# Optimization experiments

Measured on AMD Instinct MI355X. Metric: run time of the kernel, lower is better.

## Reference

```python
import jax, jax.numpy as jnp
import numpy as np

B, T, D, H = 2, 2048, 1024, 16

def setup_inputs() -> dict:
    key = jax.random.key(0)
    k0, k1, k2, k3 = jax.random.split(key, 4)
    s = 0.02
    return {
        "x": jax.random.normal(k0, (B, T, D), dtype=jnp.float32),
        "Wqkv": jax.random.normal(k1, (3 * D, D), dtype=jnp.float32) * s,
        "Wout": jax.random.normal(k2, (D, D), dtype=jnp.float32) * s,
        "bout": jax.random.normal(k3, (D,), dtype=jnp.float32) * s,
    }

def reference(x, Wqkv, Wout, bout):
    b, t, d = x.shape
    h = H
    dh = d // h
    qkv = x @ Wqkv.T  # [b,t,3d]
    q, k, v = jnp.split(qkv, 3, axis=-1)
    def merge_heads(z):
        return z.reshape(b, t, h, dh).transpose(0, 2, 1, 3)  # [b,h,t,dh]
    q, k, v = map(merge_heads, (q, k, v))
    scale = dh ** -0.5
    dots = jnp.einsum('bhid,bhjd->bhij', q, k) * scale  # [b,h,t,t]
    causal_mask = jnp.triu(jnp.ones((t, t), dtype=bool), 1)
    dots = jnp.where(causal_mask, -jnp.inf, dots)
    attn = jax.nn.softmax(dots, axis=-1)
    out = jnp.einsum('bhij,bhjd->bhid', attn, v)  # [b,h,t,dh]
    out = out.transpose(0, 2, 1, 3).reshape(b, t, d)
    return out @ Wout.T + bout
```

## Files before the change

kernel.cpp:

```cpp
#include <hip/hip_runtime.h>
#include <hip/hip_bf16.h>
#include <math.h>

typedef __bf16 bf16x8 __attribute__((ext_vector_type(8)));
typedef float f32x4 __attribute__((ext_vector_type(4)));
typedef unsigned short u16;
typedef unsigned int u32;

#define EXP2F(x) __builtin_amdgcn_exp2f(x)

constexpr int Bz = 2, T = 2048, D = 1024, H = 16;
constexpr int M = Bz * T;
constexpr int NQKV = 3 * D;
constexpr float SCALE2 = 0.125f * 1.44269504089f;

#define GLD_LDS16(g, l) __builtin_amdgcn_global_load_lds( \
    (__attribute__((address_space(1))) void*)(g),          \
    (__attribute__((address_space(3))) void*)(l), 16, 0, 0)

__global__ void f32_to_bf16_kernel(const float* __restrict__ in,
                                   u16* __restrict__ out, int n4) {
  int i = blockIdx.x * blockDim.x + threadIdx.x;
  int stride = gridDim.x * blockDim.x;
  for (; i < n4; i += stride) {
    float4 f = ((const float4*)in)[i];
    ushort4 u;
    u.x = __builtin_bit_cast(u16, (__bf16)f.x);
    u.y = __builtin_bit_cast(u16, (__bf16)f.y);
    u.z = __builtin_bit_cast(u16, (__bf16)f.z);
    u.w = __builtin_bit_cast(u16, (__bf16)f.w);
    ((ushort4*)out)[i] = u;
  }
}

template <bool FP32OUT, bool QSCALE>
__global__ __launch_bounds__(256, 2)
void gemm_bt(const u16* __restrict__ A, const u16* __restrict__ Bm,
             u16* __restrict__ outb, float* __restrict__ outf,
             const float* __restrict__ bias, int K, int ldc) {
  __shared__ __align__(16) u16 sA[128 * 64];
  __shared__ __align__(16) u16 sB[128 * 64];
  const int tid = threadIdx.x;
  const int lane = tid & 63;
  const int wid = tid >> 6;
  const int wr = wid >> 1, wc = wid & 1;

  const int nwg = gridDim.x * gridDim.y;
  const int flat = blockIdx.y * gridDim.x + blockIdx.x;
  const int cpx = nwg >> 3;
  const int swz = (flat & 7) * cpx + (flat >> 3);
  const int bx = swz % gridDim.x;
  const int by = swz / gridDim.x;

  const int row0 = by * 128;
  const int col0 = bx * 128;

  f32x4 acc[4][4];
#pragma unroll
  for (int m = 0; m < 4; ++m)
#pragma unroll
    for (int n = 0; n < 4; ++n) acc[m][n] = (f32x4){0.f, 0.f, 0.f, 0.f};

  const int nk = K >> 6;
  for (int kt = 0; kt < nk; ++kt) {
    const int k0 = kt << 6;
#pragma unroll
    for (int i = 0; i < 4; ++i) {
      int off = i * 4096 + tid * 16;
      int r = off >> 7;
      int cs = (off >> 4) & 7;
      int c = cs ^ (r & 7);
      const u16* ga = A + (size_t)(row0 + r) * K + k0 + c * 8;
      const u16* gb = Bm + (size_t)(col0 + r) * K + k0 + c * 8;
      u16* la = sA + (i * 4096 + (tid & ~63) * 16) / 2;
      u16* lb = sB + (i * 4096 + (tid & ~63) * 16) / 2;
      GLD_LDS16(ga, la);
      GLD_LDS16(gb, lb);
    }
    __syncthreads();
#pragma unroll
    for (int kk = 0; kk < 2; ++kk) {
      bf16x8 af[4], bfv[4];
#pragma unroll
      for (int m = 0; m < 4; ++m) {
        int r = wr * 64 + m * 16 + (lane & 15);
        int cs = (kk * 4 + (lane >> 4)) ^ (r & 7);
        af[m] = *(const bf16x8*)(sA + r * 64 + cs * 8);
      }
#pragma unroll
      for (int n = 0; n < 4; ++n) {
        int r = wc * 64 + n * 16 + (lane & 15);
        int cs = (kk * 4 + (lane >> 4)) ^ (r & 7);
        bfv[n] = *(const bf16x8*)(sB + r * 64 + cs * 8);
      }
#pragma unroll
      for (int m = 0; m < 4; ++m)
#pragma unroll
        for (int n = 0; n < 4; ++n)
          acc[m][n] = __builtin_amdgcn_mfma_f32_16x16x32_bf16(
              af[m], bfv[n], acc[m][n], 0, 0, 0);
    }
    __syncthreads();
  }

  const int orow0 = row0 + wr * 64;
  const int ocol0 = col0 + wc * 64;
#pragma unroll
  for (int m = 0; m < 4; ++m)
#pragma unroll
    for (int n = 0; n < 4; ++n)
#pragma unroll
      for (int j = 0; j < 4; ++j) {
        int rr = orow0 + m * 16 + (lane >> 4) * 4 + j;
        int cc = ocol0 + n * 16 + (lane & 15);
        if (FP32OUT) {
          outf[(size_t)rr * ldc + cc] = acc[m][n][j] + bias[cc];
        } else {
          float v = acc[m][n][j];
          if (QSCALE && cc < D) v *= SCALE2;
          outb[(size_t)rr * ldc + cc] = __builtin_bit_cast(u16, (__bf16)v);
        }
      }
}

__global__ __launch_bounds__(256, 3)
void flash_kernel(const u16* __restrict__ qkv, u16* __restrict__ attn_out) {
  __shared__ __align__(16) u16 sK[2][64 * 64];
  __shared__ __align__(16) u16 sVt[2][64 * 72];
  __shared__ __align__(16) u16 sP[4][16][72];

  const int tid = threadIdx.x;
  const int lane = tid & 63;
  const int l15 = lane & 15;
  const int hi = lane >> 4;
  const int w = tid >> 6;
  const int bh = blockIdx.x;
  const int b = bh >> 4, h = bh & 15;
  const int qt = (gridDim.y - 1) - blockIdx.y;
  const int q0 = qt * 64;
  const int nv = qt + 1;

  const size_t base = (size_t)b * T * 3072;
  const u16* qp = qkv + base + 0 * 1024 + h * 64;
  const u16* kp = qkv + base + 1 * 1024 + h * 64;
  const u16* vp = qkv + base + 2 * 1024 + h * 64;

  ushort4 vr[2][2];
  auto stageK = [&](u16* dst, int kt) {
#pragma unroll
    for (int i = 0; i < 2; ++i) {
      int off = i * 4096 + tid * 16;
      int r = off >> 7;
      int cs = (off >> 4) & 7;
      int c = cs ^ (r & 7);
      GLD_LDS16(kp + (size_t)(kt * 64 + r) * 3072 + c * 8,
                dst + (i * 4096 + (tid & ~63) * 16) / 2);
    }
  };
  auto loadV = [&](int kt) {
#pragma unroll
    for (int i = 0; i < 2; ++i) {
      const u16* gsrc = vp + (size_t)(kt * 64 + lane) * 3072 + (i * 4 + w) * 8;
      vr[i][0] = ((const ushort4*)gsrc)[0];
      vr[i][1] = ((const ushort4*)gsrc)[1];
    }
  };
  auto writeV = [&](u16* dst) {
#pragma unroll
    for (int i = 0; i < 2; ++i) {
      int c = i * 4 + w;
      dst[(c * 8 + 0) * 72 + lane] = vr[i][0].x;
      dst[(c * 8 + 1) * 72 + lane] = vr[i][0].y;
      dst[(c * 8 + 2) * 72 + lane] = vr[i][0].z;
      dst[(c * 8 + 3) * 72 + lane] = vr[i][0].w;
      dst[(c * 8 + 4) * 72 + lane] = vr[i][1].x;
      dst[(c * 8 + 5) * 72 + lane] = vr[i][1].y;
      dst[(c * 8 + 6) * 72 + lane] = vr[i][1].z;
      dst[(c * 8 + 7) * 72 + lane] = vr[i][1].w;
    }
  };

  bf16x8 qf[2];
#pragma unroll
  for (int kk = 0; kk < 2; ++kk)
    qf[kk] = *(const bf16x8*)(qp + (size_t)(q0 + w * 16 + l15) * 3072 +
                              kk * 32 + hi * 8);

  f32x4 o_acc[4];
#pragma unroll
  for (int n = 0; n < 4; ++n) o_acc[n] = (f32x4){0.f, 0.f, 0.f, 0.f};
  float m2 = -INFINITY, l_run = 0.f;

  stageK(sK[0], 0);
  loadV(0);
  writeV(sVt[0]);
  __syncthreads();

  for (int v = 0; v < nv; ++v) {
    const int cur = v & 1;
    const int k0 = v * 64;
    if (v + 1 < nv) {
      stageK(sK[cur ^ 1], v + 1);
      loadV(v + 1);
    }

    bf16x8 kf[2][4];
#pragma unroll
    for (int kk = 0; kk < 2; ++kk)
#pragma unroll
      for (int n = 0; n < 4; ++n) {
        int rk = n * 16 + l15;
        int cs = (kk * 4 + hi) ^ (rk & 7);
        kf[kk][n] = *(const bf16x8*)(&sK[cur][rk * 64 + cs * 8]);
      }

    f32x4 sc[4];
#pragma unroll
    for (int n = 0; n < 4; ++n) sc[n] = (f32x4){0.f, 0.f, 0.f, 0.f};
#pragma unroll
    for (int kk = 0; kk < 2; ++kk)
#pragma unroll
      for (int n = 0; n < 4; ++n)
        sc[n] = __builtin_amdgcn_mfma_f32_16x16x32_bf16(kf[kk][n], qf[kk],
                                                        sc[n], 0, 0, 0);

    const bool diag = (v == nv - 1);
    const int qrow = q0 + w * 16 + l15;
    float mx = -INFINITY;
#pragma unroll
    for (int n = 0; n < 4; ++n)
#pragma unroll
      for (int r = 0; r < 4; ++r) {
        float sv = sc[n][r];
        if (diag) {
          int kpos = k0 + n * 16 + hi * 4 + r;
          if (kpos > qrow) sv = -INFINITY;
        }
        sc[n][r] = sv;
        mx = fmaxf(mx, sv);
      }
    mx = fmaxf(mx, __shfl_xor(mx, 16, 64));
    mx = fmaxf(mx, __shfl_xor(mx, 32, 64));

    const bool skip = __all(mx <= m2);
    float alpha = 1.f;
    if (!skip) {
      float mn = fmaxf(m2, mx);
      alpha = EXP2F(m2 - mn);
      m2 = mn;
    }

    float sum = 0.f;
#pragma unroll
    for (int n = 0; n < 4; ++n) {
      float p0 = EXP2F(sc[n][0] - m2);
      float p1 = EXP2F(sc[n][1] - m2);
      float p2 = EXP2F(sc[n][2] - m2);
      float p3 = EXP2F(sc[n][3] - m2);
      sum += (p0 + p1) + (p2 + p3);
      u32 w01 = ((u32)__builtin_bit_cast(u16, (__bf16)p1) << 16) |
                __builtin_bit_cast(u16, (__bf16)p0);
      u32 w23 = ((u32)__builtin_bit_cast(u16, (__bf16)p3) << 16) |
                __builtin_bit_cast(u16, (__bf16)p2);
      *(u32*)(&sP[w][l15][n * 16 + hi * 4 + 0]) = w01;
      *(u32*)(&sP[w][l15][n * 16 + hi * 4 + 2]) = w23;
    }
    sum += __shfl_xor(sum, 16, 64);
    sum += __shfl_xor(sum, 32, 64);
    l_run = l_run * alpha + sum;

    bf16x8 vf[2][4];
#pragma unroll
    for (int ks = 0; ks < 2; ++ks)
#pragma unroll
      for (int n = 0; n < 4; ++n)
        vf[ks][n] = *(const bf16x8*)(
            &sVt[cur][(n * 16 + l15) * 72 + ks * 32 + hi * 8]);

    if (!skip) {
      float ab[4];
#pragma unroll
      for (int j = 0; j < 4; ++j) ab[j] = __shfl(alpha, hi * 4 + j, 64);
#pragma unroll
      for (int n = 0; n < 4; ++n)
#pragma unroll
        for (int j = 0; j < 4; ++j) o_acc[n][j] *= ab[j];
    }
#pragma unroll
    for (int ks = 0; ks < 2; ++ks) {
      bf16x8 pf = *(const bf16x8*)(&sP[w][l15][ks * 32 + hi * 8]);
#pragma unroll
      for (int n = 0; n < 4; ++n)
        o_acc[n] = __builtin_amdgcn_mfma_f32_16x16x32_bf16(pf, vf[ks][n],
                                                           o_acc[n], 0, 0, 0);
    }

    if (v + 1 < nv) {
      writeV(sVt[cur ^ 1]);
      __syncthreads();
    }
  }

#pragma unroll
  for (int j = 0; j < 4; ++j) {
    float lj = __shfl(l_run, hi * 4 + j, 64);
    float inv = 1.f / lj;
    int row = q0 + w * 16 + hi * 4 + j;
#pragma unroll
    for (int n = 0; n < 4; ++n) {
      int cc = h * 64 + n * 16 + l15;
      attn_out[((size_t)b * T + row) * 1024 + cc] =
          __builtin_bit_cast(u16, (__bf16)(o_acc[n][j] * inv));
    }
  }
}

extern "C" void kernel_launch(void* const* d_in, const int* in_sizes, int n_in,
                              void* d_out, int out_size, void* d_ws,
                              size_t ws_size, hipStream_t stream) {
  (void)in_sizes; (void)n_in; (void)out_size; (void)ws_size;
  const float* x = (const float*)d_in[0];
  const float* Wqkv = (const float*)d_in[1];
  const float* Wout = (const float*)d_in[2];
  const float* bout = (const float*)d_in[3];
  float* out = (float*)d_out;

  char* ws = (char*)d_ws;
  u16* x_bf = (u16*)(ws + 0);
  u16* wqkv_bf = (u16*)(ws + 8388608);
  u16* wout_bf = (u16*)(ws + 14680064);
  u16* qkvb = (u16*)(ws + 16777216);
  u16* aout = (u16*)(ws + 41943040);

  f32_to_bf16_kernel<<<2048, 256, 0, stream>>>(x, x_bf, M * D / 4);
  f32_to_bf16_kernel<<<2048, 256, 0, stream>>>(Wqkv, wqkv_bf, NQKV * D / 4);
  f32_to_bf16_kernel<<<1024, 256, 0, stream>>>(Wout, wout_bf, D * D / 4);

  gemm_bt<false, true><<<dim3(NQKV / 128, M / 128), 256, 0, stream>>>(
      x_bf, wqkv_bf, qkvb, nullptr, nullptr, D, NQKV);

  flash_kernel<<<dim3(Bz * H, T / 64), 256, 0, stream>>>(qkvb, aout);

  gemm_bt<true, false><<<dim3(D / 128, M / 128), 256, 0, stream>>>(
      aout, wout_bf, nullptr, out, bout, D, D);
}
```

Before: 113.4 us.

## Fuse conversion kernels, shuffle P in registers, reorder query tiles, raise occupancy

Merges the three fp32-to-bf16 conversion launches into one kernel. In the flash kernel, the P tile is rearranged into MFMA operand layout with cross-lane shuffles instead of a round trip through LDS, and the sP buffer is removed. Query-tile order is interleaved to balance causal workload, occupancy is raised to 4 blocks per CU, and s_setprio is wrapped around the MFMA sections. The extra shuffles add VALU work and the higher occupancy target may raise register pressure.

```diff
diff --git a/kernel.cpp b/kernel.cpp
--- a/kernel.cpp
+++ b/kernel.cpp
@@ -6,6 +6,7 @@
 typedef float f32x4 __attribute__((ext_vector_type(4)));
 typedef unsigned short u16;
 typedef unsigned int u32;
+typedef u32 u32x4 __attribute__((ext_vector_type(4)));
 
 #define EXP2F(x) __builtin_amdgcn_exp2f(x)
 
@@ -18,18 +19,31 @@
     (__attribute__((address_space(1))) void*)(g),          \
     (__attribute__((address_space(3))) void*)(l), 16, 0, 0)
 
-__global__ void f32_to_bf16_kernel(const float* __restrict__ in,
-                                   u16* __restrict__ out, int n4) {
+__global__ void cvt_all_kernel(const float* __restrict__ x,
+                               const float* __restrict__ wq,
+                               const float* __restrict__ wo,
+                               u16* __restrict__ xb, u16* __restrict__ wqb,
+                               u16* __restrict__ wob) {
+  constexpr int NX = M * D / 4;
+  constexpr int NQ = NQKV * D / 4;
+  constexpr int NW = D * D / 4;
+  constexpr int TOT = NX + NQ + NW;
   int i = blockIdx.x * blockDim.x + threadIdx.x;
   int stride = gridDim.x * blockDim.x;
-  for (; i < n4; i += stride) {
-    float4 f = ((const float4*)in)[i];
+  for (; i < TOT; i += stride) {
+    const float4* src;
+    u16* dst;
+    int j;
+    if (i < NX) { src = (const float4*)x; dst = xb; j = i; }
+    else if (i < NX + NQ) { src = (const float4*)wq; dst = wqb; j = i - NX; }
+    else { src = (const float4*)wo; dst = wob; j = i - NX - NQ; }
+    float4 f = src[j];
     ushort4 u;
     u.x = __builtin_bit_cast(u16, (__bf16)f.x);
     u.y = __builtin_bit_cast(u16, (__bf16)f.y);
     u.z = __builtin_bit_cast(u16, (__bf16)f.z);
     u.w = __builtin_bit_cast(u16, (__bf16)f.w);
-    ((ushort4*)out)[i] = u;
+    ((ushort4*)dst)[j] = u;
   }
 }
 
@@ -123,11 +137,10 @@
       }
 }
 
-__global__ __launch_bounds__(256, 3)
+__global__ __launch_bounds__(256, 4)
 void flash_kernel(const u16* __restrict__ qkv, u16* __restrict__ attn_out) {
   __shared__ __align__(16) u16 sK[2][64 * 64];
   __shared__ __align__(16) u16 sVt[2][64 * 72];
-  __shared__ __align__(16) u16 sP[4][16][72];
 
   const int tid = threadIdx.x;
   const int lane = tid & 63;
@@ -136,7 +149,10 @@
   const int w = tid >> 6;
   const int bh = blockIdx.x;
   const int b = bh >> 4, h = bh & 15;
-  const int qt = (gridDim.y - 1) - blockIdx.y;
+
+  const int yj = blockIdx.y & 7, yg = blockIdx.y >> 3;
+  const int qt = (yg == 0) ? 31 - yj : (yg == 1) ? 16 + yj
+               : (yg == 2) ? 15 - yj : yj;
   const int q0 = qt * 64;
   const int nv = qt + 1;
 
@@ -196,6 +212,10 @@
   writeV(sVt[0]);
   __syncthreads();
 
+  const int idxA = l15 + 32 * (hi & 1);
+  const int idxB = idxA + 16;
+  const bool hiSel = hi >= 2;
+
   for (int v = 0; v < nv; ++v) {
     const int cur = v & 1;
     const int k0 = v * 64;
@@ -217,12 +237,14 @@
     f32x4 sc[4];
 #pragma unroll
     for (int n = 0; n < 4; ++n) sc[n] = (f32x4){0.f, 0.f, 0.f, 0.f};
+    __builtin_amdgcn_s_setprio(1);
 #pragma unroll
     for (int kk = 0; kk < 2; ++kk)
 #pragma unroll
       for (int n = 0; n < 4; ++n)
         sc[n] = __builtin_amdgcn_mfma_f32_16x16x32_bf16(kf[kk][n], qf[kk],
                                                         sc[n], 0, 0, 0);
+    __builtin_amdgcn_s_setprio(0);
 
     const bool diag = (v == nv - 1);
     const int qrow = q0 + w * 16 + l15;
@@ -251,6 +273,7 @@
     }
 
     float sum = 0.f;
+    u32 pp[4][2];
 #pragma unroll
     for (int n = 0; n < 4; ++n) {
       float p0 = EXP2F(sc[n][0] - m2);
@@ -258,17 +281,34 @@
       float p2 = EXP2F(sc[n][2] - m2);
       float p3 = EXP2F(sc[n][3] - m2);
       sum += (p0 + p1) + (p2 + p3);
-      u32 w01 = ((u32)__builtin_bit_cast(u16, (__bf16)p1) << 16) |
-                __builtin_bit_cast(u16, (__bf16)p0);
-      u32 w23 = ((u32)__builtin_bit_cast(u16, (__bf16)p3) << 16) |
-                __builtin_bit_cast(u16, (__bf16)p2);
-      *(u32*)(&sP[w][l15][n * 16 + hi * 4 + 0]) = w01;
-      *(u32*)(&sP[w][l15][n * 16 + hi * 4 + 2]) = w23;
+      pp[n][0] = ((u32)__builtin_bit_cast(u16, (__bf16)p1) << 16) |
+                 __builtin_bit_cast(u16, (__bf16)p0);
+      pp[n][1] = ((u32)__builtin_bit_cast(u16, (__bf16)p3) << 16) |
+                 __builtin_bit_cast(u16, (__bf16)p2);
     }
     sum += __shfl_xor(sum, 16, 64);
     sum += __shfl_xor(sum, 32, 64);
     l_run = l_run * alpha + sum;
 
+    bf16x8 pf[2];
+#pragma unroll
+    for (int ks = 0; ks < 2; ++ks) {
+      u32 a0 = __shfl(pp[2 * ks][0], idxA, 64);
+      u32 b0 = __shfl(pp[2 * ks + 1][0], idxA, 64);
+      u32 a1 = __shfl(pp[2 * ks][1], idxA, 64);
+      u32 b1 = __shfl(pp[2 * ks + 1][1], idxA, 64);
+      u32 a2 = __shfl(pp[2 * ks][0], idxB, 64);
+      u32 b2 = __shfl(pp[2 * ks + 1][0], idxB, 64);
+      u32 a3 = __shfl(pp[2 * ks][1], idxB, 64);
+      u32 b3 = __shfl(pp[2 * ks + 1][1], idxB, 64);
+      u32x4 t;
+      t.x = hiSel ? b0 : a0;
+      t.y = hiSel ? b1 : a1;
+      t.z = hiSel ? b2 : a2;
+      t.w = hiSel ? b3 : a3;
+      pf[ks] = __builtin_bit_cast(bf16x8, t);
+    }
+
     bf16x8 vf[2][4];
 #pragma unroll
     for (int ks = 0; ks < 2; ++ks)
@@ -286,19 +326,17 @@
 #pragma unroll
         for (int j = 0; j < 4; ++j) o_acc[n][j] *= ab[j];
     }
-#pragma unroll
-    for (int ks = 0; ks < 2; ++ks) {
-      bf16x8 pf = *(const bf16x8*)(&sP[w][l15][ks * 32 + hi * 8]);
+    __builtin_amdgcn_s_setprio(1);
+#pragma unroll
+    for (int ks = 0; ks < 2; ++ks)
 #pragma unroll
       for (int n = 0; n < 4; ++n)
-        o_acc[n] = __builtin_amdgcn_mfma_f32_16x16x32_bf16(pf, vf[ks][n],
+        o_acc[n] = __builtin_amdgcn_mfma_f32_16x16x32_bf16(pf[ks], vf[ks][n],
                                                            o_acc[n], 0, 0, 0);
-    }
-
-    if (v + 1 < nv) {
-      writeV(sVt[cur ^ 1]);
-      __syncthreads();
-    }
+    __builtin_amdgcn_s_setprio(0);
+
+    if (v + 1 < nv) writeV(sVt[cur ^ 1]);
+    if (v + 1 < nv) __syncthreads();
   }
 
 #pragma unroll
@@ -332,9 +370,8 @@
   u16* qkvb = (u16*)(ws + 16777216);
   u16* aout = (u16*)(ws + 41943040);
 
-  f32_to_bf16_kernel<<<2048, 256, 0, stream>>>(x, x_bf, M * D / 4);
-  f32_to_bf16_kernel<<<2048, 256, 0, stream>>>(Wqkv, wqkv_bf, NQKV * D / 4);
-  f32_to_bf16_kernel<<<1024, 256, 0, stream>>>(Wout, wout_bf, D * D / 4);
+  cvt_all_kernel<<<2048, 256, 0, stream>>>(x, Wqkv, Wout, x_bf, wqkv_bf,
+                                           wout_bf);
 
   gemm_bt<false, true><<<dim3(NQKV / 128, M / 128), 256, 0, stream>>>(
       x_bf, wqkv_bf, qkvb, nullptr, nullptr, D, NQKV);
```

Result: slower. 119.3 us (+5.2%).
